# Optimization experiments

Measured on AMD Instinct MI355X. Metric: run time of the kernel, lower is better.

Reference implementation:

```python
import jax, jax.numpy as jnp
import numpy as np

N = 50000      # nodes per type
E = 262144     # edges per relation
D_IN = 256; D_OUT = 256; D_ATT = 64
NEG_SLOPE = 0.2


def setup_inputs() -> dict:
    key = jax.random.key(0)
    ks = jax.random.split(key, 22)
    rn = lambda k, s, sc=0.05: jax.random.normal(k, s, jnp.float32) * sc
    ri = lambda k, s: jax.random.randint(k, s, 0, N, jnp.int32)
    return {
        "hA": jax.random.normal(ks[0], (N, D_IN), jnp.float32),
        "hB": jax.random.normal(ks[1], (N, D_IN), jnp.float32),
        "Wself": rn(ks[2], (2, D_IN, D_OUT)),
        "bself": rn(ks[3], (2, D_OUT), 0.01),
        "Wq": rn(ks[4], (2, D_OUT, D_ATT)),
        "bq": rn(ks[5], (2, D_ATT), 0.01),
        "Wk": rn(ks[6], (2, D_OUT, D_ATT)),
        "bk": rn(ks[7], (2, D_ATT), 0.01),
        "Wal": rn(ks[8], (2, D_ATT)),
        "bal": rn(ks[9], (2,), 0.01),
        "War": rn(ks[10], (2, D_ATT)),
        "bar": rn(ks[11], (2,), 0.01),
        "Wsrc": rn(ks[12], (2, D_IN, D_OUT)),
        "bsrc": rn(ks[13], (2, D_OUT), 0.01),
        "Wdst": rn(ks[14], (2, D_IN, D_OUT)),
        "bdst": rn(ks[15], (2, D_OUT), 0.01),
        "attn_v": rn(ks[16], (2, D_OUT)),
        "gbias": rn(ks[17], (2, D_OUT), 0.01),
        "eab_src": ri(ks[18], (E,)),
        "eab_dst": ri(ks[19], (E,)),
        "eba_src": ri(ks[20], (E,)),
        "eba_dst": ri(ks[21], (E,)),
    }


def _gatv2(h_src, h_dst, src, dst, Ws, bs, Wd, bd, av, gb, n_dst):
    """DGL GATv2Conv, num_heads=1: e_uv = av . leaky_relu(fc_src(h)[u] + fc_dst(h)[v]),
    edge-softmax over incoming edges per dst, message = alpha * fc_src(h)[u], + bias."""
    ft_s = h_src @ Ws + bs                              # (Ns, D)
    ft_d = h_dst @ Wd + bd                              # (Nd, D)
    e = jax.nn.leaky_relu(ft_s[src] + ft_d[dst], NEG_SLOPE)  # (E, D)
    logits = e @ av                                     # (E,)
    m = jax.ops.segment_max(logits, dst, num_segments=n_dst)
    m = jnp.where(jnp.isfinite(m), m, 0.0)              # zero-in-degree safety
    ex = jnp.exp(logits - m[dst])
    den = jax.ops.segment_sum(ex, dst, num_segments=n_dst)
    alpha = ex / jnp.where(den[dst] > 0, den[dst], 1.0)  # (E,) edge softmax
    out = jax.ops.segment_sum(alpha[:, None] * ft_s[src], dst, num_segments=n_dst) + gb
    return out, alpha


def _forward(hA, hB, Wself, bself, Wq, bq, Wk, bk, Wal, bal, War, bar,
             Wsrc, bsrc, Wdst, bdst, attn_v, gbias,
             eab_src, eab_dst, eba_src, eba_dst):
    h = [hA, hB]
    z = [h[t] @ Wself[t] + bself[t] for t in range(2)]       # HeteroLinear W_self
    q = [z[t] @ Wq[t] + bq[t] for t in range(2)]
    k = [z[t] @ Wk[t] + bk[t] for t in range(2)]
    h_l = [k[t] @ Wal[t] + bal[t] for t in range(2)]          # (N,) = W_al(key)
    h_r = [q[t] @ War[t] + bar[t] for t in range(2)]          # (N,) = W_ar(query)
    att_self = [jax.nn.elu(h_l[t] + h_r[t]) for t in range(2)]

    # relation "ab": A -> B (etype index 0)
    rst_ab, a_ab = _gatv2(hA, hB, eab_src, eab_dst,
                          Wsrc[0], bsrc[0], Wdst[0], bdst[0], attn_v[0], gbias[0], N)
    eatt_b = jax.nn.elu((rst_ab @ Wk[1] + bk[1]) @ Wal[1] + bal[1] + h_r[1])
    # relation "ba": B -> A (etype index 1)
    rst_ba, a_ba = _gatv2(hB, hA, eba_src, eba_dst,
                          Wsrc[1], bsrc[1], Wdst[1], bdst[1], attn_v[1], gbias[1], N)
    eatt_a = jax.nn.elu((rst_ba @ Wk[0] + bk[0]) @ Wal[0] + bal[0] + h_r[0])

    attA = jax.nn.softmax(jnp.stack([att_self[0], eatt_a]), axis=0)  # (2, N)
    attB = jax.nn.softmax(jnp.stack([att_self[1], eatt_b]), axis=0)
    rstA = jax.nn.elu(attA[0][:, None] * z[0] + attA[1][:, None] * rst_ba)
    rstB = jax.nn.elu(attB[0][:, None] * z[1] + attB[1][:, None] * rst_ab)
    return jnp.stack([rstA, rstB])  # (2, N, D_OUT)


def reference(hA, hB, Wself, bself, Wq, bq, Wk, bk, Wal, bal, War, bar,
              Wsrc, bsrc, Wdst, bdst, attn_v, gbias,
              eab_src, eab_dst, eba_src, eba_dst):
    return _forward(hA, hB, Wself, bself, Wq, bq, Wk, bk, Wal, bal, War, bar,
                    Wsrc, bsrc, Wdst, bdst, attn_v, gbias,
                    eab_src, eab_dst, eba_src, eba_dst)
```

## Files before the change

### kernel.cpp

```cpp
#include <hip/hip_runtime.h>
#include <math.h>

#define NNODES 50000
#define NEDGES 262144
#define NEG_SLOPE 0.2f
#define NBINS (2 * NNODES)
#define NXP 391
#define NWG_GEMM (2 * NXP * 6)

typedef __attribute__((ext_vector_type(8))) short short8;
typedef __attribute__((ext_vector_type(4))) float f32x4;
typedef __attribute__((ext_vector_type(2))) float f32x2;
typedef __attribute__((ext_vector_type(4))) unsigned short u16x4;

#define AUX_PS 0
#define AUX_PD (2 * NNODES)
#define AUX_HL (4 * NNODES)
#define AUX_HR (6 * NNODES)

__device__ __forceinline__ float elu_f(float x) { return x > 0.f ? x : (__expf(x) - 1.f); }
__device__ __forceinline__ float bf2f(unsigned short u) {
    return __uint_as_float(((unsigned)u) << 16);
}
__device__ __forceinline__ f32x2 bfp2f(unsigned p) {
    f32x2 r;
    r.x = __uint_as_float(p << 16);
    r.y = __uint_as_float(p & 0xffff0000u);
    return r;
}
__device__ __forceinline__ unsigned short f2bf(float f) {
    unsigned u = __float_as_uint(f);
    unsigned r = (u + 0x7fffu + ((u >> 16) & 1u)) >> 16;
    return (unsigned short)r;
}

__global__ __launch_bounds__(256) void conv_bf16_2(const float* __restrict__ inA,
                                                   const float* __restrict__ inB,
                                                   unsigned short* __restrict__ outA,
                                                   unsigned short* __restrict__ outB,
                                                   int half) {
    int i = (blockIdx.x * 256 + threadIdx.x) * 4;
    if (i >= 2 * half) return;
    const float* in = (i < half) ? inA : inB;
    unsigned short* out = (i < half) ? outA : outB;
    int k = (i < half) ? i : i - half;
    float4 v = *reinterpret_cast<const float4*>(&in[k]);
    u16x4 o;
    o[0] = f2bf(v.x); o[1] = f2bf(v.y); o[2] = f2bf(v.z); o[3] = f2bf(v.w);
    *reinterpret_cast<u16x4*>(&out[k]) = o;
}

__global__ __launch_bounds__(256) void prep_w(
    const float* __restrict__ Wself, const float* __restrict__ Wsrc, const float* __restrict__ Wdst,
    const float* __restrict__ bself, const float* __restrict__ bsrc, const float* __restrict__ bdst,
    unsigned short* __restrict__ Wt, float* __restrict__ biasF) {
    int r = blockIdx.x;
    int t = r / 768;
    int n = r % 768;
    int seg = n >> 8;
    int nn = n & 255;
    const float* W; const float* bv; int ti;
    if (seg == 0)      { W = Wself; bv = bself; ti = t; }
    else if (seg == 1) { W = Wsrc;  bv = bsrc;  ti = t; }
    else               { W = Wdst;  bv = bdst;  ti = 1 - t; }
    int k = threadIdx.x;
    float val = W[(size_t)ti * 65536 + (size_t)k * 256 + nn];
    Wt[(size_t)r * 256 + k] = f2bf(val);
    if (k == 0) biasF[r] = bv[ti * 256 + nn];
}

__global__ __launch_bounds__(256) void precompute_uv(
    const float* __restrict__ Wq, const float* __restrict__ bq,
    const float* __restrict__ Wk, const float* __restrict__ bk,
    const float* __restrict__ Wal, const float* __restrict__ bal,
    const float* __restrict__ War, const float* __restrict__ bar,
    float* __restrict__ u_l, float* __restrict__ u_r,
    float* __restrict__ c_l, float* __restrict__ c_r) {
    int t = blockIdx.x;
    int d = threadIdx.x;
    float sl = 0.f, sr = 0.f;
    for (int j = 0; j < 64; ++j) {
        sl += Wk[((size_t)t * 256 + d) * 64 + j] * Wal[t * 64 + j];
        sr += Wq[((size_t)t * 256 + d) * 64 + j] * War[t * 64 + j];
    }
    u_l[t * 256 + d] = sl;
    u_r[t * 256 + d] = sr;
    if (d == 0) {
        float cl = bal[t], cr = bar[t];
        for (int j = 0; j < 64; ++j) {
            cl += bk[t * 64 + j] * Wal[t * 64 + j];
            cr += bq[t * 64 + j] * War[t * 64 + j];
        }
        c_l[t] = cl; c_r[t] = cr;
    }
}

__global__ __launch_bounds__(256) void hist2(const int* __restrict__ dab,
                                             const int* __restrict__ dba,
                                             int* __restrict__ counts) {
    int e = blockIdx.x * 256 + threadIdx.x;
    if (e < NEDGES) atomicAdd(&counts[dab[e]], 1);
    else if (e < 2 * NEDGES) atomicAdd(&counts[NNODES + dba[e - NEDGES]], 1);
}

__global__ __launch_bounds__(256) void scan1(const int* __restrict__ counts,
                                             int* __restrict__ incl,
                                             int* __restrict__ bsum, int n) {
    __shared__ int s[256];
    int i = blockIdx.x * 256 + threadIdx.x;
    int t = threadIdx.x;
    s[t] = (i < n) ? counts[i] : 0;
    __syncthreads();
#pragma unroll
    for (int off = 1; off < 256; off <<= 1) {
        int x = (t >= off) ? s[t - off] : 0;
        __syncthreads();
        s[t] += x;
        __syncthreads();
    }
    if (i < n) incl[i] = s[t];
    if (t == 255) bsum[blockIdx.x] = s[255];
}

__global__ __launch_bounds__(512) void scan2(int* __restrict__ bsum, int nb) {
    __shared__ int s[512];
    int t = threadIdx.x;
    s[t] = (t < nb) ? bsum[t] : 0;
    __syncthreads();
#pragma unroll
    for (int off = 1; off < 512; off <<= 1) {
        int x = (t >= off) ? s[t - off] : 0;
        __syncthreads();
        s[t] += x;
        __syncthreads();
    }
    if (t < nb) bsum[t] = s[t];
}

__global__ __launch_bounds__(256) void scan3(const int* __restrict__ counts,
                                             int* __restrict__ incl_to_excl,
                                             const int* __restrict__ bsum,
                                             int* __restrict__ cursor, int n) {
    int i = blockIdx.x * 256 + threadIdx.x;
    if (i >= n) return;
    int base = (blockIdx.x > 0) ? bsum[blockIdx.x - 1] : 0;
    int st = base + incl_to_excl[i] - counts[i];
    incl_to_excl[i] = st;
    cursor[i] = st;
}

__global__ __launch_bounds__(256) void scatter2(const int* __restrict__ sab,
                                                const int* __restrict__ dab,
                                                const int* __restrict__ sba,
                                                const int* __restrict__ dba,
                                                int* __restrict__ cursor,
                                                int* __restrict__ sorted_src) {
    int e = blockIdx.x * 256 + threadIdx.x;
    if (e < NEDGES) {
        int pos = atomicAdd(&cursor[dab[e]], 1);
        sorted_src[pos] = sab[e];
    } else if (e < 2 * NEDGES) {
        int k = e - NEDGES;
        int pos = atomicAdd(&cursor[NNODES + dba[k]], 1);
        sorted_src[pos] = sba[k];
    }
}

__global__ __launch_bounds__(256) void gemm_mfma(
    const unsigned short* __restrict__ hAb,
    const unsigned short* __restrict__ hBb,
    const unsigned short* __restrict__ Wt,
    const float* __restrict__ biasF,
    const float* __restrict__ attn_v,
    const float* __restrict__ u_l,
    const float* __restrict__ u_r,
    unsigned short* __restrict__ bufA,
    unsigned short* __restrict__ bufB,
    float* __restrict__ aux,
    int M)
{
    __shared__ unsigned short lds[16384];
    const int tid = threadIdx.x;
    const int lane = tid & 63;
    const int w = tid >> 6;
    const int wm = w >> 1, wn = w & 1;

    const int nwg = NWG_GEMM;
    const int q = nwg / 8, r = nwg % 8;
    int orig = blockIdx.x;
    int xcd = orig % 8, idx = orig / 8;
    int wgid = (xcd < r) ? (xcd * (q + 1) + idx) : (r * (q + 1) + (xcd - r) * q + idx);
    int t   = wgid / (NXP * 6);
    int rem = wgid % (NXP * 6);
    int xp  = rem / 6;
    int yc  = rem % 6;

    const int row0 = xp * 128;
    const int col0 = yc * 128;
    const unsigned short* Ain = t ? hBb : hAb;
    const unsigned short* Wtt = Wt + (size_t)t * 768 * 256;
    const float* bias = biasF + t * 768;
    unsigned short* Cout = t ? bufB : bufA;

    f32x4 acc[4][4] = {};

    const unsigned short* gA[2];
    const unsigned short* gB[2];
#pragma unroll
    for (int rr = 0; rr < 2; ++rr) {
        int qq = rr * 256 + tid;
        int row = qq >> 2;
        int c = (qq & 3) ^ ((row >> 1) & 3);
        int ga = min(row0 + row, M - 1);
        gA[rr] = Ain + (size_t)ga * 256 + c * 8;
        gB[rr] = Wtt + (size_t)(col0 + row) * 256 + c * 8;
    }

#define STAGE(buf, kt)                                                                   \
    {                                                                                    \
        unsigned short* Ad = lds + (buf) * 4096;                                         \
        unsigned short* Bd = lds + 8192 + (buf) * 4096;                                  \
        _Pragma("unroll")                                                                \
        for (int rr = 0; rr < 2; ++rr) {                                                 \
            __builtin_amdgcn_global_load_lds(                                            \
                (const __attribute__((address_space(1))) unsigned int*)(gA[rr] + (kt)),  \
                (__attribute__((address_space(3))) unsigned int*)(Ad + ((rr * 256 + w * 64) << 3)), \
                16, 0, 0);                                                               \
            __builtin_amdgcn_global_load_lds(                                            \
                (const __attribute__((address_space(1))) unsigned int*)(gB[rr] + (kt)),  \
                (__attribute__((address_space(3))) unsigned int*)(Bd + ((rr * 256 + w * 64) << 3)), \
                16, 0, 0);                                                               \
        }                                                                                \
    }

    STAGE(0, 0);
    STAGE(1, 32);

#pragma unroll
    for (int it = 0; it < 8; ++it) {
        const int cur = it & 1;
        if (it < 7) { asm volatile("s_waitcnt vmcnt(4)" ::: "memory"); }
        else        { asm volatile("s_waitcnt vmcnt(0)" ::: "memory"); }
        __builtin_amdgcn_s_barrier();
        __builtin_amdgcn_sched_barrier(0);

        const unsigned short* As = lds + cur * 4096;
        const unsigned short* Bs = lds + 8192 + cur * 4096;
        short8 a[4], b[4];
#pragma unroll
        for (int i = 0; i < 4; ++i) {
            int ar = wm * 64 + i * 16 + (lane & 15);
            a[i] = *reinterpret_cast<const short8*>(
                &As[ar * 32 + (((lane >> 4) ^ ((ar >> 1) & 3)) << 3)]);
            int br = wn * 64 + i * 16 + (lane & 15);
            b[i] = *reinterpret_cast<const short8*>(
                &Bs[br * 32 + (((lane >> 4) ^ ((br >> 1) & 3)) << 3)]);
        }
#pragma unroll
        for (int i = 0; i < 4; ++i)
#pragma unroll
            for (int j = 0; j < 4; ++j)
                acc[i][j] = __builtin_amdgcn_mfma_f32_16x16x32_bf16(a[i], b[j], acc[i][j], 0, 0, 0);

        asm volatile("s_waitcnt lgkmcnt(0)" ::: "memory");
        __builtin_amdgcn_sched_barrier(0);
        __builtin_amdgcn_s_barrier();
        if (it < 6) STAGE(cur, (it + 2) * 32);
    }
#undef STAGE

#pragma unroll
    for (int j = 0; j < 4; ++j) {
        int colg = wn * 4 + j;
        int ci = lane & 15;
        float bv = bias[col0 + colg * 16 + ci];
#pragma unroll
        for (int i = 0; i < 4; ++i) {
            int rowb = wm * 64 + i * 16 + ((lane >> 4) << 2);
#pragma unroll
            for (int v = 0; v < 4; ++v) {
                int row = rowb + v;
                int g2 = colg ^ ((row >> 2) & 3);
                lds[row * 128 + g2 * 16 + ci] = f2bf(acc[i][j][v] + bv);
            }
        }
    }
    __syncthreads();

    const int seg = yc >> 1;
    const float* avp1; float* axp1;
    const float* avp2 = nullptr; float* axp2 = nullptr;
    if (seg == 0) {
        avp1 = u_l + t * 256;            axp1 = aux + AUX_HL + (size_t)t * NNODES;
        avp2 = u_r + t * 256;            axp2 = aux + AUX_HR + (size_t)t * NNODES;
    } else if (seg == 1) {
        avp1 = attn_v + t * 256;         axp1 = aux + AUX_PS + (size_t)t * NNODES;
    } else {
        avp1 = attn_v + (1 - t) * 256;   axp1 = aux + AUX_PD + (size_t)(1 - t) * NNODES;
    }

#pragma unroll
    for (int p = 0; p < 8; ++p) {
        int idx = p * 256 + tid;
        int row = idx >> 4;
        int ch = idx & 15;
        int g2 = (ch >> 1) ^ ((row >> 2) & 3);
        int grow = row0 + row;
        bool ok = grow < M;
        short8 val = *reinterpret_cast<const short8*>(&lds[row * 128 + g2 * 16 + ((ch & 1) << 3)]);
        if (ok)
            *reinterpret_cast<short8*>(&Cout[(size_t)grow * 768 + col0 + ch * 8]) = val;
        int colb = (yc & 1) * 128 + ch * 8;
        float4 w0v = *reinterpret_cast<const float4*>(&avp1[colb]);
        float4 w1v = *reinterpret_cast<const float4*>(&avp1[colb + 4]);
        float p1 = w0v.x * bf2f((unsigned short)val[0]) + w0v.y * bf2f((unsigned short)val[1])
                 + w0v.z * bf2f((unsigned short)val[2]) + w0v.w * bf2f((unsigned short)val[3])
                 + w1v.x * bf2f((unsigned short)val[4]) + w1v.y * bf2f((unsigned short)val[5])
                 + w1v.z * bf2f((unsigned short)val[6]) + w1v.w * bf2f((unsigned short)val[7]);
        p1 += __shfl_xor(p1, 1);
        p1 += __shfl_xor(p1, 2);
        p1 += __shfl_xor(p1, 4);
        p1 += __shfl_xor(p1, 8);
        if ((tid & 15) == 0 && ok) atomicAdd(&axp1[grow], p1);
        if (avp2) {
            float4 y0 = *reinterpret_cast<const float4*>(&avp2[colb]);
            float4 y1 = *reinterpret_cast<const float4*>(&avp2[colb + 4]);
            float p2 = y0.x * bf2f((unsigned short)val[0]) + y0.y * bf2f((unsigned short)val[1])
                     + y0.z * bf2f((unsigned short)val[2]) + y0.w * bf2f((unsigned short)val[3])
                     + y1.x * bf2f((unsigned short)val[4]) + y1.y * bf2f((unsigned short)val[5])
                     + y1.z * bf2f((unsigned short)val[6]) + y1.w * bf2f((unsigned short)val[7]);
            p2 += __shfl_xor(p2, 1);
            p2 += __shfl_xor(p2, 2);
            p2 += __shfl_xor(p2, 4);
            p2 += __shfl_xor(p2, 8);
            if ((tid & 15) == 0 && ok) atomicAdd(&axp2[grow], p2);
        }
    }
}

__global__ __launch_bounds__(256) void gat_fused(
    const unsigned short* __restrict__ bufA, const unsigned short* __restrict__ bufB,
    const int* __restrict__ sorted_src, const int* __restrict__ row_start,
    const int* __restrict__ counts,
    const float* __restrict__ attn_v, const float* __restrict__ gbias,
    const float* __restrict__ u_l,
    const float* __restrict__ c_l, const float* __restrict__ c_r,
    const float* __restrict__ aux,
    float* __restrict__ out)
{
    const int tid = threadIdx.x;
    const int l = tid & 15;
    const int gBase = tid & 48;
    const int nd = blockIdx.x * 16 + (tid >> 4);
    if (nd >= 2 * NNODES) return;
    const int rel = nd >= NNODES;
    const int d = nd - rel * NNODES;
    const int td = rel ? 0 : 1;

    const unsigned short* zbuf = td ? bufB : bufA;
    const unsigned short* ftS = (rel ? bufB : bufA) + 256;
    const unsigned short* ftD = zbuf + 512;
    const float clv = c_l[td], crv = c_r[td];

    f32x2 fd2[8], av2[8];
    {
        const unsigned short* fdp = &ftD[(size_t)d * 768 + l * 16];
        uint4 d0 = *reinterpret_cast<const uint4*>(fdp);
        uint4 d1 = *reinterpret_cast<const uint4*>(fdp + 8);
        fd2[0] = bfp2f(d0.x); fd2[1] = bfp2f(d0.y); fd2[2] = bfp2f(d0.z); fd2[3] = bfp2f(d0.w);
        fd2[4] = bfp2f(d1.x); fd2[5] = bfp2f(d1.y); fd2[6] = bfp2f(d1.z); fd2[7] = bfp2f(d1.w);
        const float* avp = attn_v + rel * 256 + l * 16;
#pragma unroll
        for (int e = 0; e < 4; ++e) {
            float4 a = *reinterpret_cast<const float4*>(&avp[e * 4]);
            av2[2 * e].x = a.x; av2[2 * e].y = a.y;
            av2[2 * e + 1].x = a.z; av2[2 * e + 1].y = a.w;
        }
    }

    const float pd6 = 0.6f * aux[AUX_PD + (size_t)rel * NNODES + d];
    const float hlv = aux[AUX_HL + (size_t)td * NNODES + d] + clv;
    const float hrv = aux[AUX_HR + (size_t)td * NNODES + d] + crv;
    const float a0 = elu_f(hlv + hrv);
    const float* psb = aux + AUX_PS + (size_t)rel * NNODES;

    const int p0  = row_start[nd];
    const int cnt = counts[nd];
    float den = 0.f;
    f32x2 acc2[8];
#pragma unroll
    for (int e = 0; e < 8; ++e) { acc2[e].x = 0.f; acc2[e].y = 0.f; }

    for (int base = 0; base < cnt; base += 16) {
        int nloc = min(16, cnt - base);
        int sv = 0; float psl = 0.f;
        if (base + l < cnt) { sv = sorted_src[p0 + base + l]; psl = psb[sv]; }
        int j = 0;
        for (; j + 2 <= nloc; j += 2) {
            int s0 = __shfl(sv, gBase + j);
            int s1 = __shfl(sv, gBase + j + 1);
            float q0 = __shfl(psl, gBase + j);
            float q1 = __shfl(psl, gBase + j + 1);
            const unsigned short* rp0 = &ftS[(size_t)s0 * 768 + l * 16];
            const unsigned short* rp1 = &ftS[(size_t)s1 * 768 + l * 16];
            uint4 A0 = *reinterpret_cast<const uint4*>(rp0);
            uint4 A1 = *reinterpret_cast<const uint4*>(rp0 + 8);
            uint4 B0 = *reinterpret_cast<const uint4*>(rp1);
            uint4 B1 = *reinterpret_cast<const uint4*>(rp1 + 8);
            f32x2 fa2[8], fb2[8];
            fa2[0] = bfp2f(A0.x); fa2[1] = bfp2f(A0.y); fa2[2] = bfp2f(A0.z); fa2[3] = bfp2f(A0.w);
            fa2[4] = bfp2f(A1.x); fa2[5] = bfp2f(A1.y); fa2[6] = bfp2f(A1.z); fa2[7] = bfp2f(A1.w);
            fb2[0] = bfp2f(B0.x); fb2[1] = bfp2f(B0.y); fb2[2] = bfp2f(B0.z); fb2[3] = bfp2f(B0.w);
            fb2[4] = bfp2f(B1.x); fb2[5] = bfp2f(B1.y); fb2[6] = bfp2f(B1.z); fb2[7] = bfp2f(B1.w);
            float Sa = 0.f, Sb = 0.f;
#pragma unroll
            for (int e = 0; e < 8; ++e) {
                f32x2 xa = fa2[e] + fd2[e];
                f32x2 xb = fb2[e] + fd2[e];
                Sa += av2[e].x * fabsf(xa.x);
                Sa += av2[e].y * fabsf(xa.y);
                Sb += av2[e].x * fabsf(xb.x);
                Sb += av2[e].y * fabsf(xb.y);
            }
            Sa += __shfl_xor(Sa, 1); Sb += __shfl_xor(Sb, 1);
            Sa += __shfl_xor(Sa, 2); Sb += __shfl_xor(Sb, 2);
            Sa += __shfl_xor(Sa, 4); Sb += __shfl_xor(Sb, 4);
            Sa += __shfl_xor(Sa, 8); Sb += __shfl_xor(Sb, 8);
            float wa = __expf(fmaf(0.6f, q0, pd6) + 0.4f * Sa);
            float wb = __expf(fmaf(0.6f, q1, pd6) + 0.4f * Sb);
            den += wa + wb;
#pragma unroll
            for (int e = 0; e < 8; ++e) acc2[e] += wa * fa2[e] + wb * fb2[e];
        }
        if (j < nloc) {
            int s0 = __shfl(sv, gBase + j);
            float q0 = __shfl(psl, gBase + j);
            const unsigned short* rp0 = &ftS[(size_t)s0 * 768 + l * 16];
            uint4 A0 = *reinterpret_cast<const uint4*>(rp0);
            uint4 A1 = *reinterpret_cast<const uint4*>(rp0 + 8);
            f32x2 fa2[8];
            fa2[0] = bfp2f(A0.x); fa2[1] = bfp2f(A0.y); fa2[2] = bfp2f(A0.z); fa2[3] = bfp2f(A0.w);
            fa2[4] = bfp2f(A1.x); fa2[5] = bfp2f(A1.y); fa2[6] = bfp2f(A1.z); fa2[7] = bfp2f(A1.w);
            float Sa = 0.f;
#pragma unroll
            for (int e = 0; e < 8; ++e) {
                f32x2 xa = fa2[e] + fd2[e];
                Sa += av2[e].x * fabsf(xa.x);
                Sa += av2[e].y * fabsf(xa.y);
            }
            Sa += __shfl_xor(Sa, 1);
            Sa += __shfl_xor(Sa, 2);
            Sa += __shfl_xor(Sa, 4);
            Sa += __shfl_xor(Sa, 8);
            float wa = __expf(fmaf(0.6f, q0, pd6) + 0.4f * Sa);
            den += wa;
#pragma unroll
            for (int e = 0; e < 8; ++e) acc2[e] += wa * fa2[e];
        }
    }

    float inv = den > 0.f ? 1.f / den : 1.f;
    const float* gb = gbias + rel * 256 + l * 16;
    const float* ulp = u_l + td * 256 + l * 16;
    f32x2 v2[8];
    float dotv = 0.f;
#pragma unroll
    for (int e = 0; e < 4; ++e) {
        float4 g = *reinterpret_cast<const float4*>(&gb[e * 4]);
        float4 u = *reinterpret_cast<const float4*>(&ulp[e * 4]);
        v2[2 * e].x     = acc2[2 * e].x     * inv + g.x;
        v2[2 * e].y     = acc2[2 * e].y     * inv + g.y;
        v2[2 * e + 1].x = acc2[2 * e + 1].x * inv + g.z;
        v2[2 * e + 1].y = acc2[2 * e + 1].y * inv + g.w;
        dotv += v2[2 * e].x * u.x + v2[2 * e].y * u.y
              + v2[2 * e + 1].x * u.z + v2[2 * e + 1].y * u.w;
    }
    dotv += __shfl_xor(dotv, 1);
    dotv += __shfl_xor(dotv, 2);
    dotv += __shfl_xor(dotv, 4);
    dotv += __shfl_xor(dotv, 8);
    const float ea = elu_f(dotv + clv + hrv);

    float mx = fmaxf(a0, ea);
    float e0 = __expf(a0 - mx), e1 = __expf(ea - mx);
    float is = 1.f / (e0 + e1);
    float w0 = e0 * is, w1 = e1 * is;

    const unsigned short* zrow = zbuf + (size_t)d * 768 + l * 16;
    uint4 z0 = *reinterpret_cast<const uint4*>(zrow);
    uint4 z1 = *reinterpret_cast<const uint4*>(zrow + 8);
    f32x2 zf2[8];
    zf2[0] = bfp2f(z0.x); zf2[1] = bfp2f(z0.y); zf2[2] = bfp2f(z0.z); zf2[3] = bfp2f(z0.w);
    zf2[4] = bfp2f(z1.x); zf2[5] = bfp2f(z1.y); zf2[6] = bfp2f(z1.z); zf2[7] = bfp2f(z1.w);

    float* orow = out + ((size_t)(1 - rel) * NNODES + d) * 256 + l * 16;
#pragma unroll
    for (int e = 0; e < 4; ++e) {
        float4 o;
        o.x = elu_f(w0 * zf2[2 * e].x     + w1 * v2[2 * e].x);
        o.y = elu_f(w0 * zf2[2 * e].y     + w1 * v2[2 * e].y);
        o.z = elu_f(w0 * zf2[2 * e + 1].x + w1 * v2[2 * e + 1].x);
        o.w = elu_f(w0 * zf2[2 * e + 1].y + w1 * v2[2 * e + 1].y);
        *reinterpret_cast<float4*>(&orow[e * 4]) = o;
    }
}

extern "C" void kernel_launch(void* const* d_in, const int* in_sizes, int n_in,
                              void* d_out, int out_size, void* d_ws, size_t ws_size,
                              hipStream_t stream) {
    const float* hA     = (const float*)d_in[0];
    const float* hB     = (const float*)d_in[1];
    const float* Wself  = (const float*)d_in[2];
    const float* bself  = (const float*)d_in[3];
    const float* Wq     = (const float*)d_in[4];
    const float* bq     = (const float*)d_in[5];
    const float* Wk     = (const float*)d_in[6];
    const float* bk     = (const float*)d_in[7];
    const float* Wal    = (const float*)d_in[8];
    const float* bal    = (const float*)d_in[9];
    const float* War    = (const float*)d_in[10];
    const float* bar    = (const float*)d_in[11];
    const float* Wsrc   = (const float*)d_in[12];
    const float* bsrc   = (const float*)d_in[13];
    const float* Wdst   = (const float*)d_in[14];
    const float* bdst   = (const float*)d_in[15];
    const float* attn_v = (const float*)d_in[16];
    const float* gbias  = (const float*)d_in[17];
    const int* eab_src  = (const int*)d_in[18];
    const int* eab_dst  = (const int*)d_in[19];
    const int* eba_src  = (const int*)d_in[20];
    const int* eba_dst  = (const int*)d_in[21];
    float* out = (float*)d_out;
    char* ws = (char*)d_ws;

    const size_t SZ_BUF = (size_t)NNODES * 768 * sizeof(unsigned short);
    const size_t SZ_H   = (size_t)NNODES * 256 * sizeof(unsigned short);
    size_t off = 0;
    auto alloc = [&](size_t bytes) { void* p = ws + off; off = (off + bytes + 255) & ~(size_t)255; return p; };
    unsigned short* bufA = (unsigned short*)alloc(SZ_BUF);
    unsigned short* bufB = (unsigned short*)alloc(SZ_BUF);
    unsigned short* hAb  = (unsigned short*)alloc(SZ_H);
    unsigned short* hBb  = (unsigned short*)alloc(SZ_H);
    unsigned short* Wt   = (unsigned short*)alloc(2 * 768 * 256 * sizeof(unsigned short));
    float* biasF   = (float*)alloc(2 * 768 * sizeof(float));
    float* aux     = (float*)alloc((size_t)8 * NNODES * sizeof(float));
    int* counts    = (int*)alloc(NBINS * sizeof(int));
    int* row_start = (int*)alloc(NBINS * sizeof(int));
    int* cursor    = (int*)alloc(NBINS * sizeof(int));
    int* bsum      = (int*)alloc(512 * sizeof(int));
    int* sorted_src= (int*)alloc(2 * (size_t)NEDGES * sizeof(int));
    float* u_l     = (float*)alloc(2 * 256 * sizeof(float));
    float* u_r     = (float*)alloc(2 * 256 * sizeof(float));
    float* c_l     = (float*)alloc(2 * sizeof(float));
    float* c_r     = (float*)alloc(2 * sizeof(float));

    hipMemsetAsync(counts, 0, NBINS * sizeof(int), stream);
    hipMemsetAsync(aux, 0, (size_t)8 * NNODES * sizeof(float), stream);
    precompute_uv<<<2, 256, 0, stream>>>(Wq, bq, Wk, bk, Wal, bal, War, bar, u_l, u_r, c_l, c_r);

    const int HN = NNODES * 256;
    conv_bf16_2<<<(2 * HN / 4 + 255) / 256, 256, 0, stream>>>(hA, hB, hAb, hBb, HN);
    prep_w<<<2 * 768, 256, 0, stream>>>(Wself, Wsrc, Wdst, bself, bsrc, bdst, Wt, biasF);

    const int e2blocks = (2 * NEDGES + 255) / 256;
    hist2<<<e2blocks, 256, 0, stream>>>(eab_dst, eba_dst, counts);
    const int sblocks = (NBINS + 255) / 256;
    scan1<<<sblocks, 256, 0, stream>>>(counts, row_start, bsum, NBINS);
    scan2<<<1, 512, 0, stream>>>(bsum, sblocks);
    scan3<<<sblocks, 256, 0, stream>>>(counts, row_start, bsum, cursor, NBINS);
    scatter2<<<e2blocks, 256, 0, stream>>>(eab_src, eab_dst, eba_src, eba_dst, cursor, sorted_src);

    gemm_mfma<<<NWG_GEMM, 256, 0, stream>>>(hAb, hBb, Wt, biasF, attn_v, u_l, u_r,
                                            bufA, bufB, aux, NNODES);

    gat_fused<<<(2 * NNODES + 15) / 16, 256, 0, stream>>>(bufA, bufB, sorted_src, row_start,
                                                          counts, attn_v, gbias, u_l,
                                                          c_l, c_r, aux, out);
}
```

Before: 272.6 us.

## Use single-wave 64x64 GEMM tiles without barriers and merge weight prep kernels

The GEMM workgroup shrinks from four waves on a 128x128 tile to one wave on a 64x64 tile, with an XCD-aware block remap. The LDS barriers are dropped because each wave now stages and consumes only its own data. The separate precompute_uv launch is folded into the weight-prep kernel to save a launch. In exchange there are four times as many blocks, each input tile is reused less so more operand traffic reaches global memory, and there are more atomic adds for the attention projections.

```diff
diff --git a/kernel.cpp b/kernel.cpp
--- a/kernel.cpp
+++ b/kernel.cpp
@@ -5,8 +5,8 @@
 #define NEDGES 262144
 #define NEG_SLOPE 0.2f
 #define NBINS (2 * NNODES)
-#define NXP 391
-#define NWG_GEMM (2 * NXP * 6)
+#define NXP64 782
+#define NWG_GEMM (2 * NXP64 * 12)
 
 typedef __attribute__((ext_vector_type(8))) short short8;
 typedef __attribute__((ext_vector_type(4))) float f32x4;
@@ -50,11 +50,37 @@
     *reinterpret_cast<u16x4*>(&out[k]) = o;
 }
 
-__global__ __launch_bounds__(256) void prep_w(
+__global__ __launch_bounds__(256) void prep_all(
     const float* __restrict__ Wself, const float* __restrict__ Wsrc, const float* __restrict__ Wdst,
     const float* __restrict__ bself, const float* __restrict__ bsrc, const float* __restrict__ bdst,
-    unsigned short* __restrict__ Wt, float* __restrict__ biasF) {
-    int r = blockIdx.x;
+    const float* __restrict__ Wq, const float* __restrict__ bq,
+    const float* __restrict__ Wk, const float* __restrict__ bk,
+    const float* __restrict__ Wal, const float* __restrict__ bal,
+    const float* __restrict__ War, const float* __restrict__ bar,
+    unsigned short* __restrict__ Wt, float* __restrict__ biasF,
+    float* __restrict__ u_l, float* __restrict__ u_r,
+    float* __restrict__ c_l, float* __restrict__ c_r) {
+    if (blockIdx.x < 2) {
+        int t = blockIdx.x;
+        int d = threadIdx.x;
+        float sl = 0.f, sr = 0.f;
+        for (int j = 0; j < 64; ++j) {
+            sl += Wk[((size_t)t * 256 + d) * 64 + j] * Wal[t * 64 + j];
+            sr += Wq[((size_t)t * 256 + d) * 64 + j] * War[t * 64 + j];
+        }
+        u_l[t * 256 + d] = sl;
+        u_r[t * 256 + d] = sr;
+        if (d == 0) {
+            float cl = bal[t], cr = bar[t];
+            for (int j = 0; j < 64; ++j) {
+                cl += bk[t * 64 + j] * Wal[t * 64 + j];
+                cr += bq[t * 64 + j] * War[t * 64 + j];
+            }
+            c_l[t] = cl; c_r[t] = cr;
+        }
+        return;
+    }
+    int r = blockIdx.x - 2;
     int t = r / 768;
     int n = r % 768;
     int seg = n >> 8;
@@ -67,32 +93,6 @@
     float val = W[(size_t)ti * 65536 + (size_t)k * 256 + nn];
     Wt[(size_t)r * 256 + k] = f2bf(val);
     if (k == 0) biasF[r] = bv[ti * 256 + nn];
-}
-
-__global__ __launch_bounds__(256) void precompute_uv(
-    const float* __restrict__ Wq, const float* __restrict__ bq,
-    const float* __restrict__ Wk, const float* __restrict__ bk,
-    const float* __restrict__ Wal, const float* __restrict__ bal,
-    const float* __restrict__ War, const float* __restrict__ bar,
-    float* __restrict__ u_l, float* __restrict__ u_r,
-    float* __restrict__ c_l, float* __restrict__ c_r) {
-    int t = blockIdx.x;
-    int d = threadIdx.x;
-    float sl = 0.f, sr = 0.f;
-    for (int j = 0; j < 64; ++j) {
-        sl += Wk[((size_t)t * 256 + d) * 64 + j] * Wal[t * 64 + j];
-        sr += Wq[((size_t)t * 256 + d) * 64 + j] * War[t * 64 + j];
-    }
-    u_l[t * 256 + d] = sl;
-    u_r[t * 256 + d] = sr;
-    if (d == 0) {
-        float cl = bal[t], cr = bar[t];
-        for (int j = 0; j < 64; ++j) {
-            cl += bk[t * 64 + j] * Wal[t * 64 + j];
-            cr += bq[t * 64 + j] * War[t * 64 + j];
-        }
-        c_l[t] = cl; c_r[t] = cr;
-    }
 }
 
 __global__ __launch_bounds__(256) void hist2(const int* __restrict__ dab,
@@ -166,7 +166,7 @@
     }
 }
 
-__global__ __launch_bounds__(256) void gemm_mfma(
+__global__ __launch_bounds__(64) void gemm_mfma(
     const unsigned short* __restrict__ hAb,
     const unsigned short* __restrict__ hBb,
     const unsigned short* __restrict__ Wt,
@@ -179,24 +179,19 @@
     float* __restrict__ aux,
     int M)
 {
-    __shared__ unsigned short lds[16384];
-    const int tid = threadIdx.x;
-    const int lane = tid & 63;
-    const int w = tid >> 6;
-    const int wm = w >> 1, wn = w & 1;
-
-    const int nwg = NWG_GEMM;
-    const int q = nwg / 8, r = nwg % 8;
+    __shared__ unsigned short lds[8192];
+    const int lane = threadIdx.x;
+
+    const int cpx = NWG_GEMM / 8;
     int orig = blockIdx.x;
-    int xcd = orig % 8, idx = orig / 8;
-    int wgid = (xcd < r) ? (xcd * (q + 1) + idx) : (r * (q + 1) + (xcd - r) * q + idx);
-    int t   = wgid / (NXP * 6);
-    int rem = wgid % (NXP * 6);
-    int xp  = rem / 6;
-    int yc  = rem % 6;
-
-    const int row0 = xp * 128;
-    const int col0 = yc * 128;
+    int wgid = (orig & 7) * cpx + (orig >> 3);
+    int t   = wgid / (NXP64 * 12);
+    int rem = wgid % (NXP64 * 12);
+    int xp  = rem / 12;
+    int yc  = rem % 12;
+
+    const int row0 = xp * 64;
+    const int col0 = yc * 64;
     const unsigned short* Ain = t ? hBb : hAb;
     const unsigned short* Wtt = Wt + (size_t)t * 768 * 256;
     const float* bias = biasF + t * 768;
@@ -204,31 +199,31 @@
 
     f32x4 acc[4][4] = {};
 
-    const unsigned short* gA[2];
-    const unsigned short* gB[2];
-#pragma unroll
-    for (int rr = 0; rr < 2; ++rr) {
-        int qq = rr * 256 + tid;
-        int row = qq >> 2;
-        int c = (qq & 3) ^ ((row >> 1) & 3);
+    const unsigned short* gA[4];
+    const unsigned short* gB[4];
+#pragma unroll
+    for (int rr = 0; rr < 4; ++rr) {
+        int c = rr * 64 + lane;
+        int row = c >> 2;
+        int kc = (c & 3) ^ ((row >> 1) & 3);
         int ga = min(row0 + row, M - 1);
-        gA[rr] = Ain + (size_t)ga * 256 + c * 8;
-        gB[rr] = Wtt + (size_t)(col0 + row) * 256 + c * 8;
+        gA[rr] = Ain + (size_t)ga * 256 + kc * 8;
+        gB[rr] = Wtt + (size_t)(col0 + row) * 256 + kc * 8;
     }
 
 #define STAGE(buf, kt)                                                                   \
     {                                                                                    \
-        unsigned short* Ad = lds + (buf) * 4096;                                         \
-        unsigned short* Bd = lds + 8192 + (buf) * 4096;                                  \
+        unsigned short* Ad = lds + (buf) * 2048;                                         \
+        unsigned short* Bd = lds + 4096 + (buf) * 2048;                                  \
         _Pragma("unroll")                                                                \
-        for (int rr = 0; rr < 2; ++rr) {                                                 \
+        for (int rr = 0; rr < 4; ++rr) {                                                 \
             __builtin_amdgcn_global_load_lds(                                            \
                 (const __attribute__((address_space(1))) unsigned int*)(gA[rr] + (kt)),  \
-                (__attribute__((address_space(3))) unsigned int*)(Ad + ((rr * 256 + w * 64) << 3)), \
+                (__attribute__((address_space(3))) unsigned int*)(Ad + rr * 512),        \
                 16, 0, 0);                                                               \
             __builtin_amdgcn_global_load_lds(                                            \
                 (const __attribute__((address_space(1))) unsigned int*)(gB[rr] + (kt)),  \
-                (__attribute__((address_space(3))) unsigned int*)(Bd + ((rr * 256 + w * 64) << 3)), \
+                (__attribute__((address_space(3))) unsigned int*)(Bd + rr * 512),        \
                 16, 0, 0);                                                               \
         }                                                                                \
     }
@@ -239,20 +234,19 @@
 #pragma unroll
     for (int it = 0; it < 8; ++it) {
         const int cur = it & 1;
-        if (it < 7) { asm volatile("s_waitcnt vmcnt(4)" ::: "memory"); }
+        if (it < 7) { asm volatile("s_waitcnt vmcnt(8)" ::: "memory"); }
         else        { asm volatile("s_waitcnt vmcnt(0)" ::: "memory"); }
-        __builtin_amdgcn_s_barrier();
         __builtin_amdgcn_sched_barrier(0);
 
-        const unsigned short* As = lds + cur * 4096;
-        const unsigned short* Bs = lds + 8192 + cur * 4096;
+        const unsigned short* As = lds + cur * 2048;
+        const unsigned short* Bs = lds + 4096 + cur * 2048;
         short8 a[4], b[4];
 #pragma unroll
         for (int i = 0; i < 4; ++i) {
-            int ar = wm * 64 + i * 16 + (lane & 15);
+            int ar = i * 16 + (lane & 15);
             a[i] = *reinterpret_cast<const short8*>(
                 &As[ar * 32 + (((lane >> 4) ^ ((ar >> 1) & 3)) << 3)]);
-            int br = wn * 64 + i * 16 + (lane & 15);
+            int br = i * 16 + (lane & 15);
             b[i] = *reinterpret_cast<const short8*>(
                 &Bs[br * 32 + (((lane >> 4) ^ ((br >> 1) & 3)) << 3)]);
         }
@@ -264,30 +258,28 @@
 
         asm volatile("s_waitcnt lgkmcnt(0)" ::: "memory");
         __builtin_amdgcn_sched_barrier(0);
-        __builtin_amdgcn_s_barrier();
         if (it < 6) STAGE(cur, (it + 2) * 32);
     }
 #undef STAGE
 
 #pragma unroll
     for (int j = 0; j < 4; ++j) {
-        int colg = wn * 4 + j;
         int ci = lane & 15;
-        float bv = bias[col0 + colg * 16 + ci];
+        float bv = bias[col0 + j * 16 + ci];
 #pragma unroll
         for (int i = 0; i < 4; ++i) {
-            int rowb = wm * 64 + i * 16 + ((lane >> 4) << 2);
+            int rowb = i * 16 + ((lane >> 4) << 2);
 #pragma unroll
             for (int v = 0; v < 4; ++v) {
                 int row = rowb + v;
-                int g2 = colg ^ ((row >> 2) & 3);
-                lds[row * 128 + g2 * 16 + ci] = f2bf(acc[i][j][v] + bv);
+                int g2 = j ^ ((row >> 2) & 3);
+                lds[row * 64 + g2 * 16 + ci] = f2bf(acc[i][j][v] + bv);
             }
         }
     }
-    __syncthreads();
-
-    const int seg = yc >> 1;
+
+    const int seg = yc >> 2;
+    const int cq  = yc & 3;
     const float* avp1; float* axp1;
     const float* avp2 = nullptr; float* axp2 = nullptr;
     if (seg == 0) {
@@ -301,16 +293,16 @@
 
 #pragma unroll
     for (int p = 0; p < 8; ++p) {
-        int idx = p * 256 + tid;
-        int row = idx >> 4;
-        int ch = idx & 15;
+        int c = p * 64 + lane;
+        int row = c >> 3;
+        int ch = c & 7;
         int g2 = (ch >> 1) ^ ((row >> 2) & 3);
         int grow = row0 + row;
         bool ok = grow < M;
-        short8 val = *reinterpret_cast<const short8*>(&lds[row * 128 + g2 * 16 + ((ch & 1) << 3)]);
+        short8 val = *reinterpret_cast<const short8*>(&lds[row * 64 + g2 * 16 + ((ch & 1) << 3)]);
         if (ok)
             *reinterpret_cast<short8*>(&Cout[(size_t)grow * 768 + col0 + ch * 8]) = val;
-        int colb = (yc & 1) * 128 + ch * 8;
+        int colb = cq * 64 + ch * 8;
         float4 w0v = *reinterpret_cast<const float4*>(&avp1[colb]);
         float4 w1v = *reinterpret_cast<const float4*>(&avp1[colb + 4]);
         float p1 = w0v.x * bf2f((unsigned short)val[0]) + w0v.y * bf2f((unsigned short)val[1])
@@ -320,8 +312,7 @@
         p1 += __shfl_xor(p1, 1);
         p1 += __shfl_xor(p1, 2);
         p1 += __shfl_xor(p1, 4);
-        p1 += __shfl_xor(p1, 8);
-        if ((tid & 15) == 0 && ok) atomicAdd(&axp1[grow], p1);
+        if (ch == 0 && ok) atomicAdd(&axp1[grow], p1);
         if (avp2) {
             float4 y0 = *reinterpret_cast<const float4*>(&avp2[colb]);
             float4 y1 = *reinterpret_cast<const float4*>(&avp2[colb + 4]);
@@ -332,8 +323,7 @@
             p2 += __shfl_xor(p2, 1);
             p2 += __shfl_xor(p2, 2);
             p2 += __shfl_xor(p2, 4);
-            p2 += __shfl_xor(p2, 8);
-            if ((tid & 15) == 0 && ok) atomicAdd(&axp2[grow], p2);
+            if (ch == 0 && ok) atomicAdd(&axp2[grow], p2);
         }
     }
 }
@@ -556,11 +546,12 @@
 
     hipMemsetAsync(counts, 0, NBINS * sizeof(int), stream);
     hipMemsetAsync(aux, 0, (size_t)8 * NNODES * sizeof(float), stream);
-    precompute_uv<<<2, 256, 0, stream>>>(Wq, bq, Wk, bk, Wal, bal, War, bar, u_l, u_r, c_l, c_r);
 
     const int HN = NNODES * 256;
     conv_bf16_2<<<(2 * HN / 4 + 255) / 256, 256, 0, stream>>>(hA, hB, hAb, hBb, HN);
-    prep_w<<<2 * 768, 256, 0, stream>>>(Wself, Wsrc, Wdst, bself, bsrc, bdst, Wt, biasF);
+    prep_all<<<2 + 2 * 768, 256, 0, stream>>>(Wself, Wsrc, Wdst, bself, bsrc, bdst,
+                                              Wq, bq, Wk, bk, Wal, bal, War, bar,
+                                              Wt, biasF, u_l, u_r, c_l, c_r);
 
     const int e2blocks = (2 * NEDGES + 255) / 256;
     hist2<<<e2blocks, 256, 0, stream>>>(eab_dst, eba_dst, counts);
@@ -570,8 +561,8 @@
     scan3<<<sblocks, 256, 0, stream>>>(counts, row_start, bsum, cursor, NBINS);
     scatter2<<<e2blocks, 256, 0, stream>>>(eab_src, eab_dst, eba_src, eba_dst, cursor, sorted_src);
 
-    gemm_mfma<<<NWG_GEMM, 256, 0, stream>>>(hAb, hBb, Wt, biasF, attn_v, u_l, u_r,
-                                            bufA, bufB, aux, NNODES);
+    gemm_mfma<<<NWG_GEMM, 64, 0, stream>>>(hAb, hBb, Wt, biasF, attn_v, u_l, u_r,
+                                           bufA, bufB, aux, NNODES);
 
     gat_fused<<<(2 * NNODES + 15) / 16, 256, 0, stream>>>(bufA, bufB, sorted_src, row_start,
                                                           counts, attn_v, gbias, u_l,
```

Result: slower. 294.8 us (+8.1%).

## Fuse fp32-to-bf16 input conversion into GEMM A-tile loads and merge prep kernels

Applied to the files above, without the earlier changes.

The separate pass that converted hA/hB to bf16 is removed. The GEMM now loads fp32 A tiles into registers, converts them to bf16 and writes them to LDS, software-pipelined two stages ahead with adjusted vmcnt waits. The B tile still goes global-to-LDS directly. The weight-prep and u/v precompute kernels are merged into one launch. This avoids writing and re-reading a bf16 copy of the inputs (about 50 MB of traffic) and one launch, at the cost of more VGPRs, register-staged A loads, and reading fp32 A once per column tile (6x).

```diff
diff --git a/kernel.cpp b/kernel.cpp
--- a/kernel.cpp
+++ b/kernel.cpp
@@ -34,27 +34,37 @@
     return (unsigned short)r;
 }
 
-__global__ __launch_bounds__(256) void conv_bf16_2(const float* __restrict__ inA,
-                                                   const float* __restrict__ inB,
-                                                   unsigned short* __restrict__ outA,
-                                                   unsigned short* __restrict__ outB,
-                                                   int half) {
-    int i = (blockIdx.x * 256 + threadIdx.x) * 4;
-    if (i >= 2 * half) return;
-    const float* in = (i < half) ? inA : inB;
-    unsigned short* out = (i < half) ? outA : outB;
-    int k = (i < half) ? i : i - half;
-    float4 v = *reinterpret_cast<const float4*>(&in[k]);
-    u16x4 o;
-    o[0] = f2bf(v.x); o[1] = f2bf(v.y); o[2] = f2bf(v.z); o[3] = f2bf(v.w);
-    *reinterpret_cast<u16x4*>(&out[k]) = o;
-}
-
-__global__ __launch_bounds__(256) void prep_w(
+__global__ __launch_bounds__(256) void prep_all(
     const float* __restrict__ Wself, const float* __restrict__ Wsrc, const float* __restrict__ Wdst,
     const float* __restrict__ bself, const float* __restrict__ bsrc, const float* __restrict__ bdst,
-    unsigned short* __restrict__ Wt, float* __restrict__ biasF) {
-    int r = blockIdx.x;
+    const float* __restrict__ Wq, const float* __restrict__ bq,
+    const float* __restrict__ Wk, const float* __restrict__ bk,
+    const float* __restrict__ Wal, const float* __restrict__ bal,
+    const float* __restrict__ War, const float* __restrict__ bar,
+    unsigned short* __restrict__ Wt, float* __restrict__ biasF,
+    float* __restrict__ u_l, float* __restrict__ u_r,
+    float* __restrict__ c_l, float* __restrict__ c_r) {
+    if (blockIdx.x < 2) {
+        int t = blockIdx.x;
+        int d = threadIdx.x;
+        float sl = 0.f, sr = 0.f;
+        for (int j = 0; j < 64; ++j) {
+            sl += Wk[((size_t)t * 256 + d) * 64 + j] * Wal[t * 64 + j];
+            sr += Wq[((size_t)t * 256 + d) * 64 + j] * War[t * 64 + j];
+        }
+        u_l[t * 256 + d] = sl;
+        u_r[t * 256 + d] = sr;
+        if (d == 0) {
+            float cl = bal[t], cr = bar[t];
+            for (int j = 0; j < 64; ++j) {
+                cl += bk[t * 64 + j] * Wal[t * 64 + j];
+                cr += bq[t * 64 + j] * War[t * 64 + j];
+            }
+            c_l[t] = cl; c_r[t] = cr;
+        }
+        return;
+    }
+    int r = blockIdx.x - 2;
     int t = r / 768;
     int n = r % 768;
     int seg = n >> 8;
@@ -67,32 +77,6 @@
     float val = W[(size_t)ti * 65536 + (size_t)k * 256 + nn];
     Wt[(size_t)r * 256 + k] = f2bf(val);
     if (k == 0) biasF[r] = bv[ti * 256 + nn];
-}
-
-__global__ __launch_bounds__(256) void precompute_uv(
-    const float* __restrict__ Wq, const float* __restrict__ bq,
-    const float* __restrict__ Wk, const float* __restrict__ bk,
-    const float* __restrict__ Wal, const float* __restrict__ bal,
-    const float* __restrict__ War, const float* __restrict__ bar,
-    float* __restrict__ u_l, float* __restrict__ u_r,
-    float* __restrict__ c_l, float* __restrict__ c_r) {
-    int t = blockIdx.x;
-    int d = threadIdx.x;
-    float sl = 0.f, sr = 0.f;
-    for (int j = 0; j < 64; ++j) {
-        sl += Wk[((size_t)t * 256 + d) * 64 + j] * Wal[t * 64 + j];
-        sr += Wq[((size_t)t * 256 + d) * 64 + j] * War[t * 64 + j];
-    }
-    u_l[t * 256 + d] = sl;
-    u_r[t * 256 + d] = sr;
-    if (d == 0) {
-        float cl = bal[t], cr = bar[t];
-        for (int j = 0; j < 64; ++j) {
-            cl += bk[t * 64 + j] * Wal[t * 64 + j];
-            cr += bq[t * 64 + j] * War[t * 64 + j];
-        }
-        c_l[t] = cl; c_r[t] = cr;
-    }
 }
 
 __global__ __launch_bounds__(256) void hist2(const int* __restrict__ dab,
@@ -167,8 +151,8 @@
 }
 
 __global__ __launch_bounds__(256) void gemm_mfma(
-    const unsigned short* __restrict__ hAb,
-    const unsigned short* __restrict__ hBb,
+    const float* __restrict__ hA,
+    const float* __restrict__ hB,
     const unsigned short* __restrict__ Wt,
     const float* __restrict__ biasF,
     const float* __restrict__ attn_v,
@@ -197,35 +181,56 @@
 
     const int row0 = xp * 128;
     const int col0 = yc * 128;
-    const unsigned short* Ain = t ? hBb : hAb;
+    const float* Afin = t ? hB : hA;
     const unsigned short* Wtt = Wt + (size_t)t * 768 * 256;
     const float* bias = biasF + t * 768;
     unsigned short* Cout = t ? bufB : bufA;
 
     f32x4 acc[4][4] = {};
 
-    const unsigned short* gA[2];
+    const float* gAf[2];
     const unsigned short* gB[2];
 #pragma unroll
     for (int rr = 0; rr < 2; ++rr) {
         int qq = rr * 256 + tid;
         int row = qq >> 2;
-        int c = (qq & 3) ^ ((row >> 1) & 3);
+        int kc = (qq & 3) ^ ((row >> 1) & 3);
         int ga = min(row0 + row, M - 1);
-        gA[rr] = Ain + (size_t)ga * 256 + c * 8;
-        gB[rr] = Wtt + (size_t)(col0 + row) * 256 + c * 8;
-    }
-
-#define STAGE(buf, kt)                                                                   \
+        gAf[rr] = Afin + (size_t)ga * 256 + kc * 8;
+        gB[rr] = Wtt + (size_t)(col0 + row) * 256 + kc * 8;
+    }
+
+    float4 aR[2][4];
+
+#define ISSUE_A(p, kt)                                                           \
+    {                                                                            \
+        _Pragma("unroll")                                                        \
+        for (int rr = 0; rr < 2; ++rr) {                                         \
+            aR[p][2 * rr]     = *reinterpret_cast<const float4*>(gAf[rr] + (kt));     \
+            aR[p][2 * rr + 1] = *reinterpret_cast<const float4*>(gAf[rr] + (kt) + 4); \
+        }                                                                        \
+    }
+
+#define WRITE_A(p)                                                               \
+    {                                                                            \
+        unsigned short* Ad = lds + (p) * 4096;                                   \
+        _Pragma("unroll")                                                        \
+        for (int rr = 0; rr < 2; ++rr) {                                         \
+            float4 lo = aR[p][2 * rr], hi = aR[p][2 * rr + 1];                   \
+            short8 v;                                                            \
+            v[0] = (short)f2bf(lo.x); v[1] = (short)f2bf(lo.y);                  \
+            v[2] = (short)f2bf(lo.z); v[3] = (short)f2bf(lo.w);                  \
+            v[4] = (short)f2bf(hi.x); v[5] = (short)f2bf(hi.y);                  \
+            v[6] = (short)f2bf(hi.z); v[7] = (short)f2bf(hi.w);                  \
+            *reinterpret_cast<short8*>(&Ad[(rr * 256 + tid) << 3]) = v;          \
+        }                                                                        \
+    }
+
+#define STAGE_B(buf, kt)                                                                 \
     {                                                                                    \
-        unsigned short* Ad = lds + (buf) * 4096;                                         \
         unsigned short* Bd = lds + 8192 + (buf) * 4096;                                  \
         _Pragma("unroll")                                                                \
         for (int rr = 0; rr < 2; ++rr) {                                                 \
-            __builtin_amdgcn_global_load_lds(                                            \
-                (const __attribute__((address_space(1))) unsigned int*)(gA[rr] + (kt)),  \
-                (__attribute__((address_space(3))) unsigned int*)(Ad + ((rr * 256 + w * 64) << 3)), \
-                16, 0, 0);                                                               \
             __builtin_amdgcn_global_load_lds(                                            \
                 (const __attribute__((address_space(1))) unsigned int*)(gB[rr] + (kt)),  \
                 (__attribute__((address_space(3))) unsigned int*)(Bd + ((rr * 256 + w * 64) << 3)), \
@@ -233,16 +238,23 @@
         }                                                                                \
     }
 
-    STAGE(0, 0);
-    STAGE(1, 32);
+    ISSUE_A(0, 0);
+    STAGE_B(0, 0);
+    ISSUE_A(1, 32);
+    STAGE_B(1, 32);
+    asm volatile("s_waitcnt vmcnt(6)" ::: "memory");
+    WRITE_A(0);
+    asm volatile("s_waitcnt lgkmcnt(0)" ::: "memory");
 
 #pragma unroll
     for (int it = 0; it < 8; ++it) {
         const int cur = it & 1;
-        if (it < 7) { asm volatile("s_waitcnt vmcnt(4)" ::: "memory"); }
+        if (it < 7) { asm volatile("s_waitcnt vmcnt(6)" ::: "memory"); }
         else        { asm volatile("s_waitcnt vmcnt(0)" ::: "memory"); }
         __builtin_amdgcn_s_barrier();
         __builtin_amdgcn_sched_barrier(0);
+
+        if (it < 6) ISSUE_A(cur, (it + 2) * 32);
 
         const unsigned short* As = lds + cur * 4096;
         const unsigned short* Bs = lds + 8192 + cur * 4096;
@@ -265,9 +277,19 @@
         asm volatile("s_waitcnt lgkmcnt(0)" ::: "memory");
         __builtin_amdgcn_sched_barrier(0);
         __builtin_amdgcn_s_barrier();
-        if (it < 6) STAGE(cur, (it + 2) * 32);
-    }
-#undef STAGE
+
+        if (it < 7) {
+            if (it < 6) { asm volatile("s_waitcnt vmcnt(6)" ::: "memory"); }
+            else        { asm volatile("s_waitcnt vmcnt(2)" ::: "memory"); }
+            __builtin_amdgcn_sched_barrier(0);
+            WRITE_A(cur ^ 1);
+            if (it < 6) STAGE_B(cur, (it + 2) * 32);
+            asm volatile("s_waitcnt lgkmcnt(0)" ::: "memory");
+        }
+    }
+#undef ISSUE_A
+#undef WRITE_A
+#undef STAGE_B
 
 #pragma unroll
     for (int j = 0; j < 4; ++j) {
@@ -534,13 +556,10 @@
     char* ws = (char*)d_ws;
 
     const size_t SZ_BUF = (size_t)NNODES * 768 * sizeof(unsigned short);
-    const size_t SZ_H   = (size_t)NNODES * 256 * sizeof(unsigned short);
     size_t off = 0;
     auto alloc = [&](size_t bytes) { void* p = ws + off; off = (off + bytes + 255) & ~(size_t)255; return p; };
     unsigned short* bufA = (unsigned short*)alloc(SZ_BUF);
     unsigned short* bufB = (unsigned short*)alloc(SZ_BUF);
-    unsigned short* hAb  = (unsigned short*)alloc(SZ_H);
-    unsigned short* hBb  = (unsigned short*)alloc(SZ_H);
     unsigned short* Wt   = (unsigned short*)alloc(2 * 768 * 256 * sizeof(unsigned short));
     float* biasF   = (float*)alloc(2 * 768 * sizeof(float));
     float* aux     = (float*)alloc((size_t)8 * NNODES * sizeof(float));
@@ -556,11 +575,10 @@
 
     hipMemsetAsync(counts, 0, NBINS * sizeof(int), stream);
     hipMemsetAsync(aux, 0, (size_t)8 * NNODES * sizeof(float), stream);
-    precompute_uv<<<2, 256, 0, stream>>>(Wq, bq, Wk, bk, Wal, bal, War, bar, u_l, u_r, c_l, c_r);
-
-    const int HN = NNODES * 256;
-    conv_bf16_2<<<(2 * HN / 4 + 255) / 256, 256, 0, stream>>>(hA, hB, hAb, hBb, HN);
-    prep_w<<<2 * 768, 256, 0, stream>>>(Wself, Wsrc, Wdst, bself, bsrc, bdst, Wt, biasF);
+
+    prep_all<<<2 + 2 * 768, 256, 0, stream>>>(Wself, Wsrc, Wdst, bself, bsrc, bdst,
+                                              Wq, bq, Wk, bk, Wal, bal, War, bar,
+                                              Wt, biasF, u_l, u_r, c_l, c_r);
 
     const int e2blocks = (2 * NEDGES + 255) / 256;
     hist2<<<e2blocks, 256, 0, stream>>>(eab_dst, eba_dst, counts);
@@ -570,7 +588,7 @@
     scan3<<<sblocks, 256, 0, stream>>>(counts, row_start, bsum, cursor, NBINS);
     scatter2<<<e2blocks, 256, 0, stream>>>(eab_src, eab_dst, eba_src, eba_dst, cursor, sorted_src);
 
-    gemm_mfma<<<NWG_GEMM, 256, 0, stream>>>(hAb, hBb, Wt, biasF, attn_v, u_l, u_r,
+    gemm_mfma<<<NWG_GEMM, 256, 0, stream>>>(hA, hB, Wt, biasF, attn_v, u_l, u_r,
                                             bufA, bufB, aux, NNODES);
 
     gat_fused<<<(2 * NNODES + 15) / 16, 256, 0, stream>>>(bufA, bufB, sorted_src, row_start,
```

New measurement: 282.1 us. 1.03x slower.
